# Kernel optimization log

Measured on AMD Instinct MI355X. Metric: run time of the kernel, lower is better.

Reference implementation:

```python
import jax, jax.numpy as jnp
import numpy as np

B, DIM, HEADS, HW = 32, 384, 8, 48
CH = DIM // HEADS  # 48 channels per head


def pool_matrix(H, s):
    # PyTorch AdaptiveAvgPool2d binning: start=floor(i*H/s), end=ceil((i+1)*H/s)
    P = np.zeros((s, H), np.float32)
    for i in range(s):
        a = (i * H) // s
        b = -((-(i + 1) * H) // s)
        P[i, a:b] = 1.0 / (b - a)
    return jnp.asarray(P)


def dwconv(x, w, b, p):
    # depthwise conv, NCHW, kernel [C,1,k,k], stride 1, symmetric pad p
    y = jax.lax.conv_general_dilated(
        x, w, (1, 1), [(p, p), (p, p)],
        dimension_numbers=('NCHW', 'OIHW', 'NCHW'),
        feature_group_count=x.shape[1])
    if b is not None:
        y = y + b[None, :, None, None]
    return y


def setup_inputs() -> dict:
    key = jax.random.key(0)
    ks = jax.random.split(key, 10)
    s = 0.02
    return {
        'x': jax.random.normal(ks[0], (B, DIM, HW, HW), jnp.float32),
        'ln_w': jnp.ones((DIM,), jnp.float32),
        'ln_b': jnp.zeros((DIM,), jnp.float32),
        'w_qkv': jax.random.normal(ks[1], (3 * DIM, DIM), jnp.float32) * s,
        'w_dw': jax.random.normal(ks[2], (3 * DIM, 1, 3, 3), jnp.float32) * s,
        'temperature': jnp.ones((HEADS, 1, 1), jnp.float32),
        'conv3_w': jax.random.normal(ks[3], (3 * CH, 1, 3, 3), jnp.float32) * s,
        'conv3_b': jnp.zeros((3 * CH,), jnp.float32),
        'conv5_w': jax.random.normal(ks[4], (3 * CH, 1, 5, 5), jnp.float32) * s,
        'conv5_b': jnp.zeros((3 * CH,), jnp.float32),
        'conv7_w': jax.random.normal(ks[5], (2 * CH, 1, 7, 7), jnp.float32) * s,
        'conv7_b': jnp.zeros((2 * CH,), jnp.float32),
        'w_proj': jax.random.normal(ks[6], (DIM, DIM), jnp.float32) * s,
    }


def reference(x, ln_w, ln_b, w_qkv, w_dw, temperature,
              conv3_w, conv3_b, conv5_w, conv5_b, conv7_w, conv7_b, w_proj):
    b, C, H, W = x.shape
    heads, Ch = HEADS, C // HEADS
    N = H * W
    # WithBias LayerNorm over channel dim (biased variance, eps 1e-5)
    mu = x.mean(axis=1, keepdims=True)
    var = ((x - mu) ** 2).mean(axis=1, keepdims=True)
    xn = (x - mu) / jnp.sqrt(var + 1e-5) * ln_w[None, :, None, None] + ln_b[None, :, None, None]
    # qkv: 1x1 conv then depthwise 3x3 (groups = 3*dim)
    qkv = jnp.einsum('bchw,oc->bohw', xn, w_qkv)
    qkv = dwconv(qkv, w_dw, None, 1)
    q, k, v = jnp.split(qkv, 3, axis=1)
    q = q.reshape(b, heads, Ch, N)
    k = k.reshape(b, heads, Ch, N)
    v = v.reshape(b, heads, Ch, N)
    # L2-normalize along token dim (F.normalize eps=1e-12)
    qn = q / jnp.maximum(jnp.linalg.norm(q, axis=-1, keepdims=True), 1e-12)
    kn = k / jnp.maximum(jnp.linalg.norm(k, axis=-1, keepdims=True), 1e-12)
    # channel attention [b,h,Ch,Ch]
    attn = jax.nn.relu(jnp.einsum('bhcn,bhdn->bhcd', qn, kn) * temperature[None])
    # ---- FilterModule (crpe) ----
    v_img = v.reshape(b, heads * Ch, H, W)
    # low-pass: 4 equal channel chunks, adaptive avg pool to (1,3,5,7), bilinear up
    chunk = (heads * Ch) // 4
    lp_parts = []
    for idx, sz in enumerate((1, 3, 5, 7)):
        part = v_img[:, idx * chunk:(idx + 1) * chunk]
        Pr = pool_matrix(H, sz)
        Pc = pool_matrix(W, sz)
        pooled = jnp.einsum('ph,bchw,qw->bcpq', Pr, part, Pc)
        lp_parts.append(jax.image.resize(pooled, (b, chunk, H, W), method='linear'))
    LP = jax.nn.relu(jnp.concatenate(lp_parts, axis=1))
    # high-pass: grouped depthwise convs on [3Ch, 3Ch, 2Ch] channel splits
    s0, s1 = 3 * Ch, 3 * Ch
    HP = jnp.concatenate([
        dwconv(v_img[:, :s0], conv3_w, conv3_b, 1),
        dwconv(v_img[:, s0:s0 + s1], conv5_w, conv5_b, 2),
        dwconv(v_img[:, s0 + s1:], conv7_w, conv7_b, 3),
    ], axis=1)
    HP = HP.reshape(b, heads, Ch, N)
    LPf = LP.reshape(b, heads, Ch, N)
    crpe = qn * HP + LPf
    # ---- output ----
    out = jnp.einsum('bhcd,bhdn->bhcn', attn, v)
    out = (Ch ** -0.5) * out + crpe
    out = out.reshape(b, C, H, W)
    out = jnp.einsum('bchw,oc->bohw', out, w_proj)
    return out
```

## Files before the change

### kernel.cpp

```cpp
#include <hip/hip_runtime.h>

typedef unsigned short u16;
typedef short sh4 __attribute__((ext_vector_type(4)));
typedef short short8 __attribute__((ext_vector_type(8)));
typedef u16 ush8 __attribute__((ext_vector_type(8)));
typedef __bf16 bf16x8 __attribute__((ext_vector_type(8)));
typedef float f32x4 __attribute__((ext_vector_type(4)));

#define NB 32
#define CDIM 384
#define NSP 2304
#define QCH 1152

__device__ __forceinline__ float b2f(u16 u) {
    union { unsigned i; float f; } v; v.i = ((unsigned)u) << 16; return v.f;
}
__device__ __forceinline__ u16 f2b(float f) {
    union { float f; unsigned i; } v; v.f = f;
    unsigned r = v.i + 0x7FFFu + ((v.i >> 16) & 1u);
    return (u16)(r >> 16);
}
__device__ __forceinline__ void gload16(const u16* g, u16* l) {
    __builtin_amdgcn_global_load_lds((const __attribute__((address_space(1))) unsigned int*)(g),
                                     (__attribute__((address_space(3))) unsigned int*)(l), 16, 0, 0);
}

__global__ __launch_bounds__(256) void k_prep(const float* __restrict__ wqkv,
                                              const float* __restrict__ wproj,
                                              u16* __restrict__ wqkv_bf,
                                              u16* __restrict__ wproj_bf) {
    int i = blockIdx.x * 256 + threadIdx.x;
    if (i < QCH * CDIM) wqkv_bf[i] = f2b(wqkv[i]);
    if (i < CDIM * CDIM) wproj_bf[i] = f2b(wproj[i]);
}

__global__ __launch_bounds__(256) void k_ln(const float* __restrict__ x,
                                            const float* __restrict__ lnw,
                                            const float* __restrict__ lnb,
                                            u16* __restrict__ xnt) {
    __shared__ float s_sum[4][64], s_sq[4][64], s_mu[64], s_rs[64];
    __shared__ u16 s_tile[64][392];
    int b = blockIdx.y, n0 = blockIdx.x * 64;
    int tid = threadIdx.x, c4 = tid >> 6, nl = tid & 63;
    int cbase = c4 * 96;
    const float* xb = x + (size_t)b * CDIM * NSP + (size_t)cbase * NSP + n0 + nl;
    float v[96];
    float sum = 0.f, sq = 0.f;
#pragma unroll
    for (int j = 0; j < 96; j++) {
        v[j] = xb[(size_t)j * NSP];
        sum += v[j]; sq += v[j] * v[j];
    }
    s_sum[c4][nl] = sum; s_sq[c4][nl] = sq;
    __syncthreads();
    if (tid < 64) {
        float s = s_sum[0][tid] + s_sum[1][tid] + s_sum[2][tid] + s_sum[3][tid];
        float q = s_sq[0][tid] + s_sq[1][tid] + s_sq[2][tid] + s_sq[3][tid];
        float mu = s * (1.f / CDIM);
        float var = q * (1.f / CDIM) - mu * mu;
        s_mu[tid] = mu; s_rs[tid] = rsqrtf(var + 1e-5f);
    }
    __syncthreads();
    float mu = s_mu[nl], rs = s_rs[nl];
#pragma unroll
    for (int j = 0; j < 96; j++) {
        int c = cbase + j;
        s_tile[nl][c] = f2b((v[j] - mu) * rs * lnw[c] + lnb[c]);
    }
    __syncthreads();
    u16* o = xnt + ((size_t)b * NSP + n0) * CDIM;
    for (int i = tid; i < 64 * 48; i += 256) {
        int row = i / 48, c8 = i % 48;
        *(short8*)(o + row * CDIM + c8 * 8) = *(const short8*)(&s_tile[row][c8 * 8]);
    }
}

__global__ __launch_bounds__(256) void k_gemm(const u16* __restrict__ A,
                                              const u16* __restrict__ Bt,
                                              void* __restrict__ Cmat, int M, int f32out) {
    __shared__ __align__(16) u16 As[128 * 64];
    __shared__ __align__(16) u16 Bs[128 * 64];
    int tid = threadIdx.x;
    int bxn = blockIdx.x, bym = blockIdx.y, bz = blockIdx.z;
    int wave = tid >> 6, lane = tid & 63, wr = wave >> 1, wc = wave & 1;
    int lr = lane & 15, lk = lane >> 4;
    f32x4 acc[4][4];
#pragma unroll
    for (int m = 0; m < 4; m++)
#pragma unroll
        for (int n = 0; n < 4; n++) acc[m][n] = (f32x4){0.f, 0.f, 0.f, 0.f};
    int coloff = ((lane & 7) ^ (lane >> 3)) * 8;
    int rsub = lane >> 3;
    const u16* Ag = A + (size_t)(bym * 128 + wave * 32 + rsub) * 384 + coloff;
    const u16* Bg = Bt + ((size_t)bz * NSP + bxn * 128 + wave * 32 + rsub) * 384 + coloff;
    u16* Al = As + (wave * 4) * 512;
    u16* Bl = Bs + (wave * 4) * 512;
    for (int k0 = 0; k0 < 384; k0 += 64) {
#pragma unroll
        for (int i = 0; i < 4; i++) {
            gload16(Ag + (size_t)(i * 8) * 384 + k0, Al + i * 512);
            gload16(Bg + (size_t)(i * 8) * 384 + k0, Bl + i * 512);
        }
        __syncthreads();
        short8 bfr[4][2];
#pragma unroll
        for (int n = 0; n < 4; n++) {
            int row = wc * 64 + n * 16 + lr;
#pragma unroll
            for (int h = 0; h < 2; h++)
                bfr[n][h] = *(const short8*)(Bs + row * 64 + ((h * 4 + lk) ^ (lr & 7)) * 8);
        }
#pragma unroll
        for (int m = 0; m < 4; m++) {
            int row = wr * 64 + m * 16 + lr;
            short8 a0 = *(const short8*)(As + row * 64 + ((lk) ^ (lr & 7)) * 8);
            short8 a1 = *(const short8*)(As + row * 64 + ((4 + lk) ^ (lr & 7)) * 8);
#pragma unroll
            for (int n = 0; n < 4; n++) {
                acc[m][n] = __builtin_amdgcn_mfma_f32_16x16x32_bf16(
                    __builtin_bit_cast(bf16x8, a0), __builtin_bit_cast(bf16x8, bfr[n][0]),
                    acc[m][n], 0, 0, 0);
                acc[m][n] = __builtin_amdgcn_mfma_f32_16x16x32_bf16(
                    __builtin_bit_cast(bf16x8, a1), __builtin_bit_cast(bf16x8, bfr[n][1]),
                    acc[m][n], 0, 0, 0);
            }
        }
        __syncthreads();
    }
#pragma unroll
    for (int m = 0; m < 4; m++)
#pragma unroll
        for (int n = 0; n < 4; n++) {
            int row = bym * 128 + wr * 64 + m * 16 + lk * 4;
            int col = bxn * 128 + wc * 64 + n * 16 + lr;
            if (f32out) {
                float* cp = (float*)Cmat + ((size_t)bz * M + row) * NSP + col;
#pragma unroll
                for (int r = 0; r < 4; r++) cp[(size_t)r * NSP] = acc[m][n][r];
            } else {
                u16* cp = (u16*)Cmat + ((size_t)bz * M + row) * NSP + col;
#pragma unroll
                for (int r = 0; r < 4; r++) cp[(size_t)r * NSP] = f2b(acc[m][n][r]);
            }
        }
}

__global__ __launch_bounds__(192) void k_dw3(u16* __restrict__ qkv,
                                             const float* __restrict__ wdw,
                                             float* __restrict__ sumsq) {
    __shared__ u16 s_in[4 * 2304];
    __shared__ float s_part[192];
    int bx = blockIdx.x, b = blockIdx.y, tid = threadIdx.x;
    u16* gbase = qkv + ((size_t)b * QCH + bx * 4) * NSP;
#pragma unroll
    for (int i = 0; i < 6; i++) {
        int c = tid + i * 192;
        *(ush8*)(&s_in[c * 8]) = *(const ush8*)(gbase + c * 8);
    }
    int p = tid / 48, y = tid % 48;
    int ch = bx * 4 + p;
    float w[9];
#pragma unroll
    for (int i = 0; i < 9; i++) w[i] = wdw[ch * 9 + i];
    __syncthreads();
    const u16* L = &s_in[p * 2304];
    ush8 r0[6], r1[6], r2[6];
#pragma unroll
    for (int o = 0; o < 6; o++) {
        r1[o] = *(const ush8*)(L + y * 48 + o * 8);
        if (y > 0)  r0[o] = *(const ush8*)(L + (y - 1) * 48 + o * 8); else r0[o] = 0;
        if (y < 47) r2[o] = *(const ush8*)(L + (y + 1) * 48 + o * 8); else r2[o] = 0;
    }
    float ss = 0.f;
    short8 outv[6];
#pragma unroll
    for (int g = 0; g < 6; g++) {
        float a0[10], a1[10], a2[10];
#pragma unroll
        for (int j = 0; j < 10; j++) {
            int xi = g * 8 - 1 + j;
            if (xi < 0 || xi >= 48) { a0[j] = 0.f; a1[j] = 0.f; a2[j] = 0.f; }
            else {
                a0[j] = b2f(r0[xi >> 3][xi & 7]);
                a1[j] = b2f(r1[xi >> 3][xi & 7]);
                a2[j] = b2f(r2[xi >> 3][xi & 7]);
            }
        }
        union { u16 u[8]; short8 v; } pk;
#pragma unroll
        for (int x = 0; x < 8; x++) {
            float o = a0[x] * w[0] + a0[x + 1] * w[1] + a0[x + 2] * w[2]
                    + a1[x] * w[3] + a1[x + 1] * w[4] + a1[x + 2] * w[5]
                    + a2[x] * w[6] + a2[x + 1] * w[7] + a2[x + 2] * w[8];
            ss += o * o;
            pk.u[x] = f2b(o);
        }
        outv[g] = pk.v;
    }
    s_part[tid] = ss;
    __syncthreads();
#pragma unroll
    for (int g = 0; g < 6; g++)
        *(short8*)(&s_in[p * 2304 + y * 48 + g * 8]) = outv[g];
    __syncthreads();
#pragma unroll
    for (int i = 0; i < 6; i++) {
        int c = tid + i * 192;
        *(ush8*)(gbase + c * 8) = *(const ush8*)(&s_in[c * 8]);
    }
    if (bx < 192 && tid < 4) {
        float s = 0.f;
        for (int i = 0; i < 48; i++) s += s_part[tid * 48 + i];
        sumsq[b * 768 + bx * 4 + tid] = s;
    }
}

__global__ void k_rnorm(const float* __restrict__ ss, float* __restrict__ rn) {
    int i = blockIdx.x * 256 + threadIdx.x;
    if (i < NB * 768) rn[i] = 1.f / fmaxf(sqrtf(ss[i]), 1e-12f);
}

__global__ __launch_bounds__(512) void k_attn(const u16* __restrict__ qkv,
                                              const float* __restrict__ rn,
                                              const float* __restrict__ temp,
                                              u16* __restrict__ attn) {
    __shared__ float s_part[8][48 * 48];
    int h = blockIdx.x, b = blockIdx.y, tid = threadIdx.x;
    int wave = tid >> 6, lane = tid & 63;
    int lr = lane & 15, lk = lane >> 4;
    const u16* qp = qkv + ((size_t)b * QCH + h * 48) * NSP;
    const u16* kp = qkv + ((size_t)b * QCH + 384 + h * 48) * NSP;
    f32x4 acc[3][3];
#pragma unroll
    for (int m = 0; m < 3; m++)
#pragma unroll
        for (int n = 0; n < 3; n++) acc[m][n] = (f32x4){0.f, 0.f, 0.f, 0.f};
    int k0 = wave * 288 + lk * 8;
    short8 af[3], bf[3], afn[3], bfn[3];
#pragma unroll
    for (int m = 0; m < 3; m++) {
        af[m] = *(const short8*)(qp + (size_t)(m * 16 + lr) * NSP + k0);
        bf[m] = *(const short8*)(kp + (size_t)(m * 16 + lr) * NSP + k0);
    }
    for (int s = 0; s < 9; s++) {
        if (s < 8) {
#pragma unroll
            for (int m = 0; m < 3; m++) {
                afn[m] = *(const short8*)(qp + (size_t)(m * 16 + lr) * NSP + k0 + 32 * (s + 1));
                bfn[m] = *(const short8*)(kp + (size_t)(m * 16 + lr) * NSP + k0 + 32 * (s + 1));
            }
        }
#pragma unroll
        for (int m = 0; m < 3; m++)
#pragma unroll
            for (int n = 0; n < 3; n++)
                acc[m][n] = __builtin_amdgcn_mfma_f32_16x16x32_bf16(
                    __builtin_bit_cast(bf16x8, af[m]), __builtin_bit_cast(bf16x8, bf[n]),
                    acc[m][n], 0, 0, 0);
#pragma unroll
        for (int m = 0; m < 3; m++) { af[m] = afn[m]; bf[m] = bfn[m]; }
    }
#pragma unroll
    for (int m = 0; m < 3; m++)
#pragma unroll
        for (int n = 0; n < 3; n++)
#pragma unroll
            for (int r = 0; r < 4; r++)
                s_part[wave][(m * 16 + lk * 4 + r) * 48 + n * 16 + lr] = acc[m][n][r];
    __syncthreads();
    float th = temp[h];
    const float* rq = rn + b * 768 + h * 48;
    const float* rk = rn + b * 768 + 384 + h * 48;
    u16* ap = attn + ((size_t)(b * 8 + h)) * NSP;
    for (int f = tid; f < 2304; f += 512) {
        int c = f / 48, d = f % 48;
        float v = 0.f;
#pragma unroll
        for (int wv = 0; wv < 8; wv++) v += s_part[wv][f];
        v *= th * rq[c] * rk[d];
        ap[f] = f2b(fmaxf(v, 0.f));
    }
}

template<int KS, int CH0, int NCH>
__global__ __launch_bounds__(256) void k_hp_t(const u16* __restrict__ qkv,
                                              const float* __restrict__ wk,
                                              const float* __restrict__ bk,
                                              u16* __restrict__ hp) {
    constexpr int PAD = KS / 2;
    constexpr int NIN = 8 + 2 * PAD;
    int t = blockIdx.x * 256 + threadIdx.x;
    int y = t % 48;
    int rem = t / 48;
    int chl = rem % NCH;
    int b = rem / NCH;
    int ch = CH0 + chl;
    const u16* src = qkv + ((size_t)b * QCH + 768 + ch) * NSP;
    float bias = bk[chl];
    float acc[48];
#pragma unroll
    for (int i = 0; i < 48; i++) acc[i] = bias;
    for (int dy = 0; dy < KS; dy++) {
        int yy = y - PAD + dy;
        if (yy < 0 || yy >= 48) continue;
        ush8 r[6];
#pragma unroll
        for (int o = 0; o < 6; o++) r[o] = *(const ush8*)(src + yy * 48 + o * 8);
        float wr[KS];
#pragma unroll
        for (int dx = 0; dx < KS; dx++) wr[dx] = wk[chl * KS * KS + dy * KS + dx];
#pragma unroll
        for (int g = 0; g < 6; g++) {
            float a[NIN];
#pragma unroll
            for (int j = 0; j < NIN; j++) {
                int xi = g * 8 - PAD + j;
                a[j] = (xi < 0 || xi >= 48) ? 0.f : b2f(r[xi >> 3][xi & 7]);
            }
#pragma unroll
            for (int x = 0; x < 8; x++) {
                float s = 0.f;
#pragma unroll
                for (int dx = 0; dx < KS; dx++) s += a[x + dx] * wr[dx];
                acc[g * 8 + x] += s;
            }
        }
    }
    u16* dst = hp + ((size_t)b * CDIM + ch) * NSP + y * 48;
#pragma unroll
    for (int g = 0; g < 6; g++) {
        union { u16 u[8]; short8 v; } pk;
#pragma unroll
        for (int x = 0; x < 8; x++) pk.u[x] = f2b(acc[g * 8 + x]);
        *(short8*)(dst + g * 8) = pk.v;
    }
}

__global__ __launch_bounds__(64) void k_pool(const u16* __restrict__ qkv,
                                             float* __restrict__ pooled) {
    int c = blockIdx.x, b = blockIdx.y, tid = threadIdx.x;
    int s = 2 * (c / 96) + 1;
    __shared__ u16 s_p[2304];
    __shared__ float rp[48][7];
    const u16* src = qkv + ((size_t)b * QCH + 768 + c) * NSP;
    for (int f = tid; f < 288; f += 64)
        *(ush8*)(&s_p[f * 8]) = *(const ush8*)(src + f * 8);
    __syncthreads();
    if (tid < 48) {
        for (int q = 0; q < s; q++) {
            int a = q * 48 / s, e = ((q + 1) * 48 + s - 1) / s;
            float sum = 0.f;
            for (int xx = a; xx < e; xx++) sum += b2f(s_p[tid * 48 + xx]);
            rp[tid][q] = sum / (float)(e - a);
        }
    }
    __syncthreads();
    if (tid < s * s) {
        int p = tid / s, q = tid % s;
        int a = p * 48 / s, e = ((p + 1) * 48 + s - 1) / s;
        float sum = 0.f;
        for (int r = a; r < e; r++) sum += rp[r][q];
        pooled[((size_t)b * CDIM + c) * 49 + tid] = sum / (float)(e - a);
    }
}

__global__ __launch_bounds__(256) void k_out(const u16* __restrict__ qkv,
                                             const u16* __restrict__ attn,
                                             const float* __restrict__ rn,
                                             const u16* __restrict__ hp,
                                             const float* __restrict__ pooled,
                                             u16* __restrict__ tmpt) {
    int nc = blockIdx.x, h = blockIdx.y, b = blockIdx.z, tid = threadIdx.x;
    __shared__ u16 s_at[48 * 72];
    __shared__ u16 s_vt[64 * 72];
    __shared__ float s_pool[48][49];
    __shared__ float s_rq[48];
    int n0 = nc * 64;
    for (int f = tid; f < 432; f += 256) *(ush8*)(&s_at[f * 8]) = (ush8)0;
    for (int f = tid; f < 576; f += 256) *(ush8*)(&s_vt[f * 8]) = (ush8)0;
    __syncthreads();
    const u16* ag = attn + ((size_t)(b * 8 + h)) * NSP;
    for (int f = tid; f < 288; f += 256) {
        int c = f / 6, j = f % 6;
        *(ush8*)(&s_at[c * 72 + j * 8]) = *(const ush8*)(ag + c * 48 + j * 8);
    }
    const u16* vsrc = qkv + ((size_t)b * QCH + 768 + h * 48) * NSP + n0;
    for (int f = tid; f < 3072; f += 256) {
        int d = f >> 6, nn = f & 63;
        s_vt[nn * 72 + d] = vsrc[(size_t)d * NSP + nn];
    }
    for (int f = tid; f < 48 * 49; f += 256)
        s_pool[f / 49][f % 49] = pooled[((size_t)b * CDIM + h * 48) * 49 + f];
    if (tid < 48) s_rq[tid] = rn[b * 768 + h * 48 + tid];
    __syncthreads();
    int wave = tid >> 6, lane = tid & 63, lr = lane & 15, lk = lane >> 4;
    f32x4 acc[3];
#pragma unroll
    for (int m = 0; m < 3; m++) acc[m] = (f32x4){0.f, 0.f, 0.f, 0.f};
#pragma unroll
    for (int ks = 0; ks < 2; ks++) {
        short8 bfr = *(const short8*)(&s_vt[(wave * 16 + lr) * 72 + ks * 32 + lk * 8]);
#pragma unroll
        for (int m = 0; m < 3; m++) {
            short8 af = *(const short8*)(&s_at[(m * 16 + lr) * 72 + ks * 32 + lk * 8]);
            acc[m] = __builtin_amdgcn_mfma_f32_16x16x32_bf16(
                __builtin_bit_cast(bf16x8, af), __builtin_bit_cast(bf16x8, bfr),
                acc[m], 0, 0, 0);
        }
    }
    int s = 2 * (h / 2) + 1;
    const float inv = 0.14433756729740643f;
    int n = n0 + wave * 16 + lr;
    int y = n / 48, xx = n % 48;
    float syf = (y + 0.5f) * s * (1.f / 48.f) - 0.5f;
    int iy0 = (int)floorf(syf); float fy = syf - (float)iy0;
    int iy1 = min(iy0 + 1, s - 1); iy0 = max(iy0, 0);
    float sxf = (xx + 0.5f) * s * (1.f / 48.f) - 0.5f;
    int ix0 = (int)floorf(sxf); float fx = sxf - (float)ix0;
    int ix1 = min(ix0 + 1, s - 1); ix0 = max(ix0, 0);
    const u16* qp = qkv + ((size_t)b * QCH + h * 48) * NSP + n;
    const u16* hq = hp + ((size_t)b * CDIM + h * 48) * NSP + n;
    u16* tp = tmpt + ((size_t)b * NSP + n) * CDIM + h * 48;
#pragma unroll
    for (int m = 0; m < 3; m++) {
        int cb = m * 16 + lk * 4;
        union { u16 u[4]; sh4 v; } pk;
#pragma unroll
        for (int r = 0; r < 4; r++) {
            int ch = cb + r;
            float qv = b2f(qp[(size_t)ch * NSP]);
            float hv = b2f(hq[(size_t)ch * NSP]);
            const float* P = s_pool[ch];
            float lp = (1.f - fy) * ((1.f - fx) * P[iy0 * s + ix0] + fx * P[iy0 * s + ix1])
                     + fy * ((1.f - fx) * P[iy1 * s + ix0] + fx * P[iy1 * s + ix1]);
            lp = fmaxf(lp, 0.f);
            pk.u[r] = f2b(inv * acc[m][r] + qv * s_rq[ch] * hv + lp);
        }
        *(sh4*)(tp + cb) = pk.v;
    }
}

extern "C" void kernel_launch(void* const* d_in, const int* in_sizes, int n_in,
                              void* d_out, int out_size, void* d_ws, size_t ws_size,
                              hipStream_t stream) {
    const float* x    = (const float*)d_in[0];
    const float* lnw  = (const float*)d_in[1];
    const float* lnb  = (const float*)d_in[2];
    const float* wqkv = (const float*)d_in[3];
    const float* wdw  = (const float*)d_in[4];
    const float* temp = (const float*)d_in[5];
    const float* w3   = (const float*)d_in[6];
    const float* b3   = (const float*)d_in[7];
    const float* w5   = (const float*)d_in[8];
    const float* b5   = (const float*)d_in[9];
    const float* w7   = (const float*)d_in[10];
    const float* b7   = (const float*)d_in[11];
    const float* wproj= (const float*)d_in[12];
    float* out = (float*)d_out;

    char* w = (char*)d_ws;
    const size_t SZ_XNT = (size_t)NB * NSP * CDIM * 2;
    const size_t SZ_QKV = (size_t)NB * QCH * NSP * 2;
    u16* xnt      = (u16*)w;
    u16* qkvb     = (u16*)(w + SZ_XNT);
    u16* hpb      = (u16*)(w + SZ_XNT + SZ_QKV);
    char* tail    = w + SZ_XNT + SZ_QKV + (size_t)NB * CDIM * NSP * 2;
    float* sumsq  = (float*)tail;
    float* rnorm  = sumsq + NB * 768;
    u16*  attnb   = (u16*)(rnorm + NB * 768);
    float* pooled = (float*)(attnb + (size_t)NB * 8 * NSP);
    u16* wqkv_bf  = (u16*)(pooled + (size_t)NB * CDIM * 49);
    u16* wproj_bf = wqkv_bf + (size_t)QCH * CDIM;
    u16* tmpt = xnt;

    k_prep <<<dim3((QCH * CDIM + 255) / 256), 256, 0, stream>>>(wqkv, wproj, wqkv_bf, wproj_bf);
    k_ln   <<<dim3(36, NB), 256, 0, stream>>>(x, lnw, lnb, xnt);
    k_gemm <<<dim3(18, 9, NB), 256, 0, stream>>>(wqkv_bf, xnt, qkvb, QCH, 0);
    k_dw3  <<<dim3(288, NB), 192, 0, stream>>>(qkvb, wdw, sumsq);
    k_rnorm<<<dim3(96), 256, 0, stream>>>(sumsq, rnorm);
    k_attn <<<dim3(8, NB), 512, 0, stream>>>(qkvb, rnorm, temp, attnb);
    k_hp_t<3, 0, 144>   <<<dim3(864), 256, 0, stream>>>(qkvb, w3, b3, hpb);
    k_hp_t<5, 144, 144> <<<dim3(864), 256, 0, stream>>>(qkvb, w5, b5, hpb);
    k_hp_t<7, 288, 96>  <<<dim3(576), 256, 0, stream>>>(qkvb, w7, b7, hpb);
    k_pool <<<dim3(CDIM, NB), 64, 0, stream>>>(qkvb, pooled);
    k_out  <<<dim3(36, 8, NB), 256, 0, stream>>>(qkvb, attnb, rnorm, hpb, pooled, tmpt);
    k_gemm <<<dim3(18, 3, NB), 256, 0, stream>>>(wproj_bf, tmpt, out, CDIM, 1);
}
```

Measured before the change: 460.3 us.

## Fold rnorm into consumers, merge high-pass conv launches, stage k_out operands in LDS

Removes the separate reciprocal-norm kernel and computes 1/max(sqrt(sumsq),eps) inline in k_attn and k_out. The three templated depthwise high-pass conv launches become a single kernel that dispatches on block index. k_out now loads its q and hp tiles into shared memory with vectorized coalesced reads instead of strided scalar global loads, copies only the s*s pooled values it needs, and skips the bilinear math when s==1. This cuts launch overhead and global memory traffic, at the cost of extra shared memory per block in k_out, which may reduce occupancy.

```diff
diff --git a/kernel.cpp b/kernel.cpp
--- a/kernel.cpp
+++ b/kernel.cpp
@@ -215,13 +215,8 @@
     }
 }
 
-__global__ void k_rnorm(const float* __restrict__ ss, float* __restrict__ rn) {
-    int i = blockIdx.x * 256 + threadIdx.x;
-    if (i < NB * 768) rn[i] = 1.f / fmaxf(sqrtf(ss[i]), 1e-12f);
-}
-
 __global__ __launch_bounds__(512) void k_attn(const u16* __restrict__ qkv,
-                                              const float* __restrict__ rn,
+                                              const float* __restrict__ sumsq,
                                               const float* __restrict__ temp,
                                               u16* __restrict__ attn) {
     __shared__ float s_part[8][48 * 48];
@@ -269,27 +264,29 @@
                 s_part[wave][(m * 16 + lk * 4 + r) * 48 + n * 16 + lr] = acc[m][n][r];
     __syncthreads();
     float th = temp[h];
-    const float* rq = rn + b * 768 + h * 48;
-    const float* rk = rn + b * 768 + 384 + h * 48;
+    const float* sqv = sumsq + b * 768 + h * 48;
+    const float* skv = sumsq + b * 768 + 384 + h * 48;
     u16* ap = attn + ((size_t)(b * 8 + h)) * NSP;
     for (int f = tid; f < 2304; f += 512) {
         int c = f / 48, d = f % 48;
         float v = 0.f;
 #pragma unroll
         for (int wv = 0; wv < 8; wv++) v += s_part[wv][f];
-        v *= th * rq[c] * rk[d];
+        float rq = 1.f / fmaxf(sqrtf(sqv[c]), 1e-12f);
+        float rk = 1.f / fmaxf(sqrtf(skv[d]), 1e-12f);
+        v *= th * rq * rk;
         ap[f] = f2b(fmaxf(v, 0.f));
     }
 }
 
 template<int KS, int CH0, int NCH>
-__global__ __launch_bounds__(256) void k_hp_t(const u16* __restrict__ qkv,
-                                              const float* __restrict__ wk,
-                                              const float* __restrict__ bk,
-                                              u16* __restrict__ hp) {
+__device__ __forceinline__ void hp_body(int g, const u16* __restrict__ qkv,
+                                        const float* __restrict__ wk,
+                                        const float* __restrict__ bk,
+                                        u16* __restrict__ hp) {
     constexpr int PAD = KS / 2;
     constexpr int NIN = 8 + 2 * PAD;
-    int t = blockIdx.x * 256 + threadIdx.x;
+    int t = g * 256 + threadIdx.x;
     int y = t % 48;
     int rem = t / 48;
     int chl = rem % NCH;
@@ -310,11 +307,11 @@
 #pragma unroll
         for (int dx = 0; dx < KS; dx++) wr[dx] = wk[chl * KS * KS + dy * KS + dx];
 #pragma unroll
-        for (int g = 0; g < 6; g++) {
+        for (int g2 = 0; g2 < 6; g2++) {
             float a[NIN];
 #pragma unroll
             for (int j = 0; j < NIN; j++) {
-                int xi = g * 8 - PAD + j;
+                int xi = g2 * 8 - PAD + j;
                 a[j] = (xi < 0 || xi >= 48) ? 0.f : b2f(r[xi >> 3][xi & 7]);
             }
 #pragma unroll
@@ -322,18 +319,29 @@
                 float s = 0.f;
 #pragma unroll
                 for (int dx = 0; dx < KS; dx++) s += a[x + dx] * wr[dx];
-                acc[g * 8 + x] += s;
+                acc[g2 * 8 + x] += s;
             }
         }
     }
     u16* dst = hp + ((size_t)b * CDIM + ch) * NSP + y * 48;
 #pragma unroll
-    for (int g = 0; g < 6; g++) {
+    for (int g2 = 0; g2 < 6; g2++) {
         union { u16 u[8]; short8 v; } pk;
 #pragma unroll
-        for (int x = 0; x < 8; x++) pk.u[x] = f2b(acc[g * 8 + x]);
-        *(short8*)(dst + g * 8) = pk.v;
-    }
+        for (int x = 0; x < 8; x++) pk.u[x] = f2b(acc[g2 * 8 + x]);
+        *(short8*)(dst + g2 * 8) = pk.v;
+    }
+}
+
+__global__ __launch_bounds__(256) void k_hp(const u16* __restrict__ qkv,
+                                            const float* __restrict__ w3, const float* __restrict__ b3,
+                                            const float* __restrict__ w5, const float* __restrict__ b5,
+                                            const float* __restrict__ w7, const float* __restrict__ b7,
+                                            u16* __restrict__ hp) {
+    int g = blockIdx.x;
+    if (g < 864)       hp_body<3, 0, 144>(g, qkv, w3, b3, hp);
+    else if (g < 1728) hp_body<5, 144, 144>(g - 864, qkv, w5, b5, hp);
+    else               hp_body<7, 288, 96>(g - 1728, qkv, w7, b7, hp);
 }
 
 __global__ __launch_bounds__(64) void k_pool(const u16* __restrict__ qkv,
@@ -366,16 +374,19 @@
 
 __global__ __launch_bounds__(256) void k_out(const u16* __restrict__ qkv,
                                              const u16* __restrict__ attn,
-                                             const float* __restrict__ rn,
+                                             const float* __restrict__ sumsq,
                                              const u16* __restrict__ hp,
                                              const float* __restrict__ pooled,
                                              u16* __restrict__ tmpt) {
     int nc = blockIdx.x, h = blockIdx.y, b = blockIdx.z, tid = threadIdx.x;
     __shared__ u16 s_at[48 * 72];
     __shared__ u16 s_vt[64 * 72];
-    __shared__ float s_pool[48][49];
+    __shared__ u16 s_q[48 * 72];
+    __shared__ u16 s_hp[48 * 72];
+    __shared__ float s_pool[48 * 49];
     __shared__ float s_rq[48];
     int n0 = nc * 64;
+    int s = 2 * (h / 2) + 1, ss2 = s * s;
     for (int f = tid; f < 432; f += 256) *(ush8*)(&s_at[f * 8]) = (ush8)0;
     for (int f = tid; f < 576; f += 256) *(ush8*)(&s_vt[f * 8]) = (ush8)0;
     __syncthreads();
@@ -389,9 +400,22 @@
         int d = f >> 6, nn = f & 63;
         s_vt[nn * 72 + d] = vsrc[(size_t)d * NSP + nn];
     }
-    for (int f = tid; f < 48 * 49; f += 256)
-        s_pool[f / 49][f % 49] = pooled[((size_t)b * CDIM + h * 48) * 49 + f];
-    if (tid < 48) s_rq[tid] = rn[b * 768 + h * 48 + tid];
+    const u16* qsrc = qkv + ((size_t)b * QCH + h * 48) * NSP + n0;
+    const u16* hsrc = hp + ((size_t)b * CDIM + h * 48) * NSP + n0;
+    for (int f = tid; f < 384; f += 256) {
+        int d = f >> 3, nn8 = (f & 7) * 8;
+        *(ush8*)(&s_q[d * 72 + nn8])  = *(const ush8*)(qsrc + (size_t)d * NSP + nn8);
+        *(ush8*)(&s_hp[d * 72 + nn8]) = *(const ush8*)(hsrc + (size_t)d * NSP + nn8);
+    }
+    const float* psrc = pooled + ((size_t)b * CDIM + h * 48) * 49;
+    for (int f = tid; f < 48 * ss2; f += 256) {
+        int c = f / ss2, idx = f - c * ss2;
+        s_pool[c * 49 + idx] = psrc[c * 49 + idx];
+    }
+    if (tid < 48) {
+        float sq_ = sumsq[b * 768 + h * 48 + tid];
+        s_rq[tid] = 1.f / fmaxf(sqrtf(sq_), 1e-12f);
+    }
     __syncthreads();
     int wave = tid >> 6, lane = tid & 63, lr = lane & 15, lk = lane >> 4;
     f32x4 acc[3];
@@ -408,18 +432,20 @@
                 acc[m], 0, 0, 0);
         }
     }
-    int s = 2 * (h / 2) + 1;
     const float inv = 0.14433756729740643f;
-    int n = n0 + wave * 16 + lr;
+    int nl_e = wave * 16 + lr;
+    int n = n0 + nl_e;
     int y = n / 48, xx = n % 48;
-    float syf = (y + 0.5f) * s * (1.f / 48.f) - 0.5f;
-    int iy0 = (int)floorf(syf); float fy = syf - (float)iy0;
-    int iy1 = min(iy0 + 1, s - 1); iy0 = max(iy0, 0);
-    float sxf = (xx + 0.5f) * s * (1.f / 48.f) - 0.5f;
-    int ix0 = (int)floorf(sxf); float fx = sxf - (float)ix0;
-    int ix1 = min(ix0 + 1, s - 1); ix0 = max(ix0, 0);
-    const u16* qp = qkv + ((size_t)b * QCH + h * 48) * NSP + n;
-    const u16* hq = hp + ((size_t)b * CDIM + h * 48) * NSP + n;
+    int iy0 = 0, iy1 = 0, ix0 = 0, ix1 = 0;
+    float fy = 0.f, fx = 0.f;
+    if (s > 1) {
+        float syf = (y + 0.5f) * s * (1.f / 48.f) - 0.5f;
+        iy0 = (int)floorf(syf); fy = syf - (float)iy0;
+        iy1 = min(iy0 + 1, s - 1); iy0 = max(iy0, 0);
+        float sxf = (xx + 0.5f) * s * (1.f / 48.f) - 0.5f;
+        ix0 = (int)floorf(sxf); fx = sxf - (float)ix0;
+        ix1 = min(ix0 + 1, s - 1); ix0 = max(ix0, 0);
+    }
     u16* tp = tmpt + ((size_t)b * NSP + n) * CDIM + h * 48;
 #pragma unroll
     for (int m = 0; m < 3; m++) {
@@ -428,11 +454,13 @@
 #pragma unroll
         for (int r = 0; r < 4; r++) {
             int ch = cb + r;
-            float qv = b2f(qp[(size_t)ch * NSP]);
-            float hv = b2f(hq[(size_t)ch * NSP]);
-            const float* P = s_pool[ch];
-            float lp = (1.f - fy) * ((1.f - fx) * P[iy0 * s + ix0] + fx * P[iy0 * s + ix1])
-                     + fy * ((1.f - fx) * P[iy1 * s + ix0] + fx * P[iy1 * s + ix1]);
+            float qv = b2f(s_q[ch * 72 + nl_e]);
+            float hv = b2f(s_hp[ch * 72 + nl_e]);
+            const float* P = &s_pool[ch * 49];
+            float lp;
+            if (s == 1) lp = P[0];
+            else lp = (1.f - fy) * ((1.f - fx) * P[iy0 * s + ix0] + fx * P[iy0 * s + ix1])
+                    + fy * ((1.f - fx) * P[iy1 * s + ix0] + fx * P[iy1 * s + ix1]);
             lp = fmaxf(lp, 0.f);
             pk.u[r] = f2b(inv * acc[m][r] + qv * s_rq[ch] * hv + lp);
         }
@@ -466,8 +494,7 @@
     u16* hpb      = (u16*)(w + SZ_XNT + SZ_QKV);
     char* tail    = w + SZ_XNT + SZ_QKV + (size_t)NB * CDIM * NSP * 2;
     float* sumsq  = (float*)tail;
-    float* rnorm  = sumsq + NB * 768;
-    u16*  attnb   = (u16*)(rnorm + NB * 768);
+    u16*  attnb   = (u16*)(sumsq + NB * 768);
     float* pooled = (float*)(attnb + (size_t)NB * 8 * NSP);
     u16* wqkv_bf  = (u16*)(pooled + (size_t)NB * CDIM * 49);
     u16* wproj_bf = wqkv_bf + (size_t)QCH * CDIM;
@@ -477,12 +504,9 @@
     k_ln   <<<dim3(36, NB), 256, 0, stream>>>(x, lnw, lnb, xnt);
     k_gemm <<<dim3(18, 9, NB), 256, 0, stream>>>(wqkv_bf, xnt, qkvb, QCH, 0);
     k_dw3  <<<dim3(288, NB), 192, 0, stream>>>(qkvb, wdw, sumsq);
-    k_rnorm<<<dim3(96), 256, 0, stream>>>(sumsq, rnorm);
-    k_attn <<<dim3(8, NB), 512, 0, stream>>>(qkvb, rnorm, temp, attnb);
-    k_hp_t<3, 0, 144>   <<<dim3(864), 256, 0, stream>>>(qkvb, w3, b3, hpb);
-    k_hp_t<5, 144, 144> <<<dim3(864), 256, 0, stream>>>(qkvb, w5, b5, hpb);
-    k_hp_t<7, 288, 96>  <<<dim3(576), 256, 0, stream>>>(qkvb, w7, b7, hpb);
+    k_attn <<<dim3(8, NB), 512, 0, stream>>>(qkvb, sumsq, temp, attnb);
+    k_hp   <<<dim3(2304), 256, 0, stream>>>(qkvb, w3, b3, w5, b5, w7, b7, hpb);
     k_pool <<<dim3(CDIM, NB), 64, 0, stream>>>(qkvb, pooled);
-    k_out  <<<dim3(36, 8, NB), 256, 0, stream>>>(qkvb, attnb, rnorm, hpb, pooled, tmpt);
+    k_out  <<<dim3(36, 8, NB), 256, 0, stream>>>(qkvb, attnb, sumsq, hpb, pooled, tmpt);
     k_gemm <<<dim3(18, 3, NB), 256, 0, stream>>>(wproj_bf, tmpt, out, CDIM, 1);
 }
```

Measured after the change: 442.0 us. -4.0%, faster.
